# Optimization experiments

Measured on AMD Instinct MI355X. Metric: run time of the kernel, lower is better.

## Reference

```python
import jax, jax.numpy as jnp
import numpy as np


def setup_inputs() -> dict:
    key = jax.random.key(0)
    k1, k2 = jax.random.split(key)
    B, C, T = 8, 256, 2048
    n_q, bins = 8, 1024
    x = jax.random.normal(k1, (B, C, T), dtype=jnp.float32)
    codebook = jax.random.normal(k2, (n_q, bins, C), dtype=jnp.float32)
    return {"x": x, "codebook": codebook, "sample_rate": 24000, "bandwidth": 6}


def reference(x, codebook, sample_rate, bandwidth):
    B, C, T = x.shape
    n_q, bins, _ = codebook.shape
    # flatten frames: (B, C, T) -> (B*T, C)
    x_flat = jnp.transpose(x, (0, 2, 1)).reshape(-1, C)
    # the expanded (N, n_q, bins, C) subtraction, without materializing it)
    x2 = jnp.sum(x_flat * x_flat, axis=-1)[:, None, None]          # (N, 1, 1)
    c2 = jnp.sum(codebook * codebook, axis=-1)[None]               # (1, n_q, bins)
    xc = jnp.einsum('nd,qbd->nqb', x_flat, codebook)               # (N, n_q, bins)
    distances = x2 + c2 - 2.0 * xc
    indices = jnp.argmin(distances, axis=-1)                       # (N, n_q)
    # gather one code per quantizer level and sum (matches the python loop)
    gathered = codebook[jnp.arange(n_q)[None, :], indices]         # (N, n_q, C)
    quant_flat = jnp.sum(gathered, axis=1)                         # (N, C)
    quantized = jnp.transpose(quant_flat.reshape(B, T, C), (0, 2, 1))
    commitment_loss = jnp.mean((jax.lax.stop_gradient(quantized) - x) ** 2)
    codebook_loss = jnp.mean((quantized - jax.lax.stop_gradient(x)) ** 2)
    loss = commitment_loss + codebook_loss
    q_ste = x + jax.lax.stop_gradient(quantized - x)               # straight-through
    return q_ste, indices, loss
```

## Files before the change

### kernel.cpp

```cpp
#include <hip/hip_runtime.h>

typedef unsigned long long u64;
typedef unsigned int u32;
typedef _Float16 f16;
typedef f16 f16x8 __attribute__((ext_vector_type(8)));
typedef float f32x4 __attribute__((ext_vector_type(4)));

#define B_   8
#define C_   256
#define T_   2048
#define NQ   8
#define BINS 1024
#define NROWS (B_ * T_)
#define KA   256
#define KB   256
#define NTILE 16
#define MARGIN 3.0f

#define XS_OFF   ((size_t)0)
#define CS_OFF   ((size_t)8388608)
#define XT_OFF   ((size_t)12582912)
#define C2D_OFF  ((size_t)29360128)
#define C2K_OFF  ((size_t)29425664)
#define IDXI_OFF ((size_t)29458432)

static __device__ __forceinline__ void gll16(const void* g, void* l) {
    __builtin_amdgcn_global_load_lds(
        (const __attribute__((address_space(1))) u32*)g,
        (__attribute__((address_space(3))) u32*)l, 16, 0, 0);
}

__global__ __launch_bounds__(256)
void prep_x(const float* __restrict__ x, float* __restrict__ x_t,
            f16* __restrict__ xs) {
    __shared__ float tile[64][65];
    const int tid = threadIdx.x;
    const int bid = blockIdx.x;
    const int b  = bid >> 7;
    const int c0 = ((bid >> 5) & 3) * 64;
    const int t0 = (bid & 31) * 64;
    {
        const int j = tid & 63, cg = tid >> 6;
        #pragma unroll
        for (int ii = 0; ii < 16; ++ii) {
            const int cl = cg * 16 + ii;
            tile[cl][j] = x[((size_t)(b * C_ + c0 + cl) * T_) + t0 + j];
        }
    }
    __syncthreads();
    {
        const int cl = tid & 63, tg = tid >> 6;
        #pragma unroll
        for (int jj = 0; jj < 16; ++jj) {
            const int tl = tg * 16 + jj;
            const float v = tile[cl][tl];
            const size_t n = (size_t)b * T_ + t0 + tl;
            x_t[n * C_ + c0 + cl] = v;
            xs[n * KA + c0 + cl]  = (f16)v;
        }
    }
}

struct alignas(8) H4 { f16 v[4]; };
__global__ __launch_bounds__(256)
void prep_cb_c2(const float* __restrict__ cb, f16* __restrict__ cs,
                double* __restrict__ c2d, float* __restrict__ c2k) {
    const int w    = threadIdx.x >> 6;
    const int lane = threadIdx.x & 63;
    const int code = blockIdx.x * 4 + w;
    const float4 v = *(const float4*)(cb + (size_t)code * C_ + lane * 4);
    H4 h;
    h.v[0] = (f16)v.x; h.v[1] = (f16)v.y; h.v[2] = (f16)v.z; h.v[3] = (f16)v.w;
    *(H4*)(cs + (size_t)code * KB + lane * 4) = h;
    double s = (double)v.x * v.x + (double)v.y * v.y +
               (double)v.z * v.z + (double)v.w * v.w;
    #pragma unroll
    for (int off = 32; off; off >>= 1) s += __shfl_down(s, off, 64);
    if (lane == 0) {
        c2d[code] = s;
        c2k[code] = (float)s + 1000.0f;
    }
}

__global__ __launch_bounds__(512)
void dist_kernel(const f16* __restrict__ xs, const f16* __restrict__ cs,
                 const float* __restrict__ c2k, const float* __restrict__ x_t,
                 const float* __restrict__ cb, const double* __restrict__ c2d,
                 float* __restrict__ idx_f, int* __restrict__ idx_i) {
    __shared__ f16 Bs[2][64][256];
    __shared__ u32 red[128][8];

    const int tid  = threadIdx.x;
    const int lane = tid & 63;
    const int w    = tid >> 6;
    const int wr   = w >> 2;
    const int wc   = w & 3;
    const int bid  = blockIdx.x;
    const int q    = bid & 7;
    const int rt   = bid >> 3;
    const int n0   = rt * 128;

    const int c = lane & 15;
    const int g = lane >> 4;

    f16x8 af[4][8];
    {
        const f16* pa = xs + (size_t)(n0 + wr * 64 + c) * KA + g * 8;
        #pragma unroll
        for (int m = 0; m < 4; ++m)
            #pragma unroll
            for (int kk = 0; kk < 8; ++kk)
                af[m][kk] = *(const f16x8*)(pa + m * 16 * KA + kk * 32);
    }

    const int crow0 = tid >> 5;
    const int slotl = (tid & 31) ^ (crow0 & 7);
    const f16* srcb = cs + (size_t)q * 1024 * KB + (size_t)crow0 * KB
                         + slotl * 8;
    const int dstw = w * 512;

    #define STAGE(buf, t)                                                    \
        do {                                                                 \
            f16* b0 = &Bs[buf][0][0] + dstw;                                 \
            const f16* s_ = srcb + (size_t)(t) * 64 * KB;                    \
            gll16(s_,                 b0);                                   \
            gll16(s_ + 16 * KB,       b0 + 4096);                            \
            gll16(s_ + 32 * KB,       b0 + 8192);                            \
            gll16(s_ + 48 * KB,       b0 + 12288);                           \
        } while (0)

    u32 k1[4][4], k2[4][4];
    #pragma unroll
    for (int m = 0; m < 4; ++m)
        #pragma unroll
        for (int r = 0; r < 4; ++r) { k1[m][r] = ~0u; k2[m][r] = ~0u; }

    const float* c2q = c2k + q * BINS;
    const int rowoff = (wc * 16 + c) * 256;
    const int sw = c & 7;

    STAGE(0, 0);
    __syncthreads();

    #pragma unroll 1
    for (int t = 0; t < NTILE; ++t) {
        const int buf = t & 1;
        if (t < NTILE - 1) STAGE(buf ^ 1, t + 1);

        f32x4 acc[4];
        #pragma unroll
        for (int m = 0; m < 4; ++m) {
            f32x4 z = {0.f, 0.f, 0.f, 0.f};
            acc[m] = z;
        }

        const f16* bb = &Bs[buf][0][0] + rowoff;
        #pragma unroll
        for (int half = 0; half < 2; ++half) {
            f16x8 bg[4];
            #pragma unroll
            for (int k4 = 0; k4 < 4; ++k4) {
                const int kk = half * 4 + k4;
                bg[k4] = *(const f16x8*)(bb + ((kk * 4 + g) ^ sw) * 8);
            }
            #pragma unroll
            for (int k4 = 0; k4 < 4; ++k4)
                #pragma unroll
                for (int m = 0; m < 4; ++m)
                    acc[m] = __builtin_amdgcn_mfma_f32_16x16x32_f16(
                        af[m][half * 4 + k4], bg[k4], acc[m], 0, 0, 0);
        }

        const int codeL = t * 64 + wc * 16 + c;
        const float cc = c2q[codeL];
        #pragma unroll
        for (int m = 0; m < 4; ++m)
            #pragma unroll
            for (int r = 0; r < 4; ++r) {
                const float sc = fmaf(-2.f, acc[m][r], cc);
                const u32 key = (__float_as_uint(sc) & 0xFFFFFC00u) | (u32)codeL;
                const u32 hi = k1[m][r] > key ? k1[m][r] : key;
                k1[m][r] = k1[m][r] < key ? k1[m][r] : key;
                k2[m][r] = k2[m][r] < hi ? k2[m][r] : hi;
            }

        __syncthreads();
    }
    #undef STAGE

    #pragma unroll
    for (int m = 0; m < 4; ++m)
        #pragma unroll
        for (int r = 0; r < 4; ++r) {
            u32 a1 = k1[m][r], a2 = k2[m][r];
            #pragma unroll
            for (int mask = 1; mask <= 8; mask <<= 1) {
                const u32 o1 = __shfl_xor(a1, mask, 64);
                const u32 o2 = __shfl_xor(a2, mask, 64);
                const u32 hi = a1 > o1 ? a1 : o1;
                a1 = a1 < o1 ? a1 : o1;
                const u32 lo2 = o2 < a2 ? o2 : a2;
                a2 = hi < lo2 ? hi : lo2;
            }
            if (c == 0) {
                const int rowl = wr * 64 + m * 16 + g * 4 + r;
                red[rowl][wc * 2]     = a1;
                red[rowl][wc * 2 + 1] = a2;
            }
        }
    __syncthreads();

    if (tid < 128) {
        u32 s0 = ~0u, s1 = ~0u, s2 = ~0u, s3 = ~0u;
        #pragma unroll
        for (int jj = 0; jj < 8; ++jj) {
            const u32 k = red[tid][jj];
            if (k < s0)      { s3 = s2; s2 = s1; s1 = s0; s0 = k; }
            else if (k < s1) { s3 = s2; s2 = s1; s1 = k; }
            else if (k < s2) { s3 = s2; s2 = k; }
            else if (k < s3) { s3 = k; }
        }
        const float f0 = __uint_as_float(s0 & 0xFFFFFC00u);
        const float f1 = __uint_as_float(s1 & 0xFFFFFC00u);
        red[tid][0] = s0 & 1023u;
        red[tid][1] = s1 & 1023u;
        red[tid][2] = s2 & 1023u;
        red[tid][3] = s3 & 1023u;
        red[tid][4] = (f1 - f0 <= MARGIN) ? 1u : 0u;
    }
    __syncthreads();

    {
        const int cand = lane >> 4;
        const int cg   = lane & 15;
        #pragma unroll 1
        for (int i = 0; i < 16; ++i) {
            const int rl = w * 16 + i;
            const int n  = n0 + rl;
            if (!red[rl][4]) {
                if (lane == 0) {
                    const int win = (int)red[rl][0];
                    idx_f[(size_t)n * NQ + q] = (float)win;
                    idx_i[(size_t)n * NQ + q] = win;
                }
                continue;
            }
            const int bin = (int)red[rl][cand];
            const float* xr = x_t + (size_t)n * C_ + cg * 16;
            const float* cr = cb + ((size_t)(q * BINS + bin)) * C_ + cg * 16;
            double d = 0.0;
            #pragma unroll
            for (int u = 0; u < 4; ++u) {
                const float4 xv = *(const float4*)(xr + u * 4);
                const float4 cv = *(const float4*)(cr + u * 4);
                d += (double)xv.x * cv.x + (double)xv.y * cv.y
                   + (double)xv.z * cv.z + (double)xv.w * cv.w;
            }
            #pragma unroll
            for (int off = 8; off; off >>= 1) d += __shfl_down(d, off, 16);
            const double dist = c2d[q * BINS + bin] - 2.0 * d;
            const double d0 = __shfl(dist,  0, 64);
            const double d1 = __shfl(dist, 16, 64);
            const double d2 = __shfl(dist, 32, 64);
            const double d3 = __shfl(dist, 48, 64);
            if (lane == 0) {
                const int b0 = (int)red[rl][0], b1 = (int)red[rl][1];
                const int b2 = (int)red[rl][2], b3 = (int)red[rl][3];
                double best = d0;
                int win = b0;
                if (d1 < best || (d1 == best && b1 < win)) { best = d1; win = b1; }
                if (d2 < best || (d2 == best && b2 < win)) { best = d2; win = b2; }
                if (d3 < best || (d3 == best && b3 < win)) { best = d3; win = b3; }
                idx_f[(size_t)n * NQ + q] = (float)win;
                idx_i[(size_t)n * NQ + q] = win;
            }
        }
    }
}

__global__ __launch_bounds__(256)
void gather_kernel(const float* __restrict__ x, const float* __restrict__ cb,
                   const int* __restrict__ idx_i, float* __restrict__ out,
                   float* __restrict__ loss) {
    __shared__ float ql[C_][17];
    const int blk = blockIdx.x;
    const int b   = blk >> 7;
    const int t0  = (blk & 127) << 4;
    const int tid = threadIdx.x;
    {
        const int c = tid;
        for (int nl = 0; nl < 16; ++nl) {
            const int n = b * T_ + t0 + nl;
            float acc = 0.f;
            #pragma unroll
            for (int qq = 0; qq < NQ; ++qq) {
                const int id = idx_i[(size_t)n * NQ + qq];
                acc += cb[((size_t)qq * BINS + id) * C_ + c];
            }
            ql[c][nl] = acc;
        }
    }
    __syncthreads();
    const int tx = tid & 15, ty = tid >> 4;
    float lsum = 0.f;
    for (int cg = 0; cg < 16; ++cg) {
        const int c = cg * 16 + ty;
        const size_t off = ((size_t)b * C_ + c) * T_ + t0 + tx;
        const float qv = ql[c][tx];
        const float xv = x[off];
        out[off] = qv;
        const float d = qv - xv;
        lsum += d * d;
    }
    #pragma unroll
    for (int off = 32; off; off >>= 1) lsum += __shfl_down(lsum, off, 64);
    if ((tid & 63) == 0)
        atomicAdd(loss, lsum * (2.0f / (float)(B_ * C_ * T_)));
}

extern "C" void kernel_launch(void* const* d_in, const int* in_sizes, int n_in,
                              void* d_out, int out_size, void* d_ws, size_t ws_size,
                              hipStream_t stream) {
    const float* x  = (const float*)d_in[0];
    const float* cb = (const float*)d_in[1];

    float* out   = (float*)d_out;
    float* idx_f = out + (size_t)B_ * C_ * T_;
    float* loss  = idx_f + (size_t)NROWS * NQ;

    char* ws = (char*)d_ws;
    f16*    xs    = (f16*)(ws + XS_OFF);
    f16*    cs    = (f16*)(ws + CS_OFF);
    float*  x_t   = (float*)(ws + XT_OFF);
    double* c2d   = (double*)(ws + C2D_OFF);
    float*  c2k   = (float*)(ws + C2K_OFF);
    int*    idx_i = (int*)(ws + IDXI_OFF);

    hipMemsetAsync(loss, 0, sizeof(float), stream);
    prep_x<<<1024, 256, 0, stream>>>(x, x_t, xs);
    prep_cb_c2<<<2048, 256, 0, stream>>>(cb, cs, c2d, c2k);
    dist_kernel<<<1024, 512, 0, stream>>>(xs, cs, c2k, x_t, cb, c2d,
                                          idx_f, idx_i);
    gather_kernel<<<B_ * (T_ / 16), 256, 0, stream>>>(x, cb, idx_i, out, loss);
}
```

Measured before the change: 231.6 us.

## Make each dist block sweep all quantizers for 64 rows with wider code tiles

The distance kernel now gives each block 64 rows and loops over all 8 quantizers' codebooks (64 tiles of 128 codes), instead of one quantizer per block over 128 rows. The x fragment is loaded into registers once and reused across all quantizers, so there are fewer redundant A loads and fewer blocks (256). Per-quantizer top-2 results are flushed to a global scratch buffer instead of shared memory. The grid shrinks to 256 blocks with 8 waves each, which may underfill the GPU's CUs. The global round-trip for the reduction data relies on __syncthreads for visibility.

```diff
diff --git a/kernel.cpp b/kernel.cpp
--- a/kernel.cpp
+++ b/kernel.cpp
@@ -14,15 +14,16 @@
 #define NROWS (B_ * T_)
 #define KA   256
 #define KB   256
-#define NTILE 16
+#define TILES 64
 #define MARGIN 3.0f
 
 #define XS_OFF   ((size_t)0)
 #define CS_OFF   ((size_t)8388608)
 #define XT_OFF   ((size_t)12582912)
-#define C2D_OFF  ((size_t)29360128)
-#define C2K_OFF  ((size_t)29425664)
-#define IDXI_OFF ((size_t)29458432)
+#define RED_OFF  ((size_t)29360128)
+#define C2D_OFF  ((size_t)37748736)
+#define C2K_OFF  ((size_t)37814272)
+#define IDXI_OFF ((size_t)37847040)
 
 static __device__ __forceinline__ void gll16(const void* g, void* l) {
     __builtin_amdgcn_global_load_lds(
@@ -82,30 +83,26 @@
     }
 }
 
-__global__ __launch_bounds__(512)
+__global__ __launch_bounds__(512, 2)
 void dist_kernel(const f16* __restrict__ xs, const f16* __restrict__ cs,
                  const float* __restrict__ c2k, const float* __restrict__ x_t,
                  const float* __restrict__ cb, const double* __restrict__ c2d,
-                 float* __restrict__ idx_f, int* __restrict__ idx_i) {
-    __shared__ f16 Bs[2][64][256];
-    __shared__ u32 red[128][8];
+                 u32* __restrict__ red_g, float* __restrict__ idx_f,
+                 int* __restrict__ idx_i) {
+    __shared__ f16 Bs[2][128][256];
 
     const int tid  = threadIdx.x;
     const int lane = tid & 63;
     const int w    = tid >> 6;
-    const int wr   = w >> 2;
-    const int wc   = w & 3;
     const int bid  = blockIdx.x;
-    const int q    = bid & 7;
-    const int rt   = bid >> 3;
-    const int n0   = rt * 128;
+    const int n0   = bid * 64;
 
     const int c = lane & 15;
     const int g = lane >> 4;
 
     f16x8 af[4][8];
     {
-        const f16* pa = xs + (size_t)(n0 + wr * 64 + c) * KA + g * 8;
+        const f16* pa = xs + (size_t)(n0 + c) * KA + g * 8;
         #pragma unroll
         for (int m = 0; m < 4; ++m)
             #pragma unroll
@@ -115,18 +112,15 @@
 
     const int crow0 = tid >> 5;
     const int slotl = (tid & 31) ^ (crow0 & 7);
-    const f16* srcb = cs + (size_t)q * 1024 * KB + (size_t)crow0 * KB
-                         + slotl * 8;
-    const int dstw = w * 512;
+    const f16* srcb = cs + (size_t)crow0 * KB + slotl * 8;
 
     #define STAGE(buf, t)                                                    \
         do {                                                                 \
-            f16* b0 = &Bs[buf][0][0] + dstw;                                 \
-            const f16* s_ = srcb + (size_t)(t) * 64 * KB;                    \
-            gll16(s_,                 b0);                                   \
-            gll16(s_ + 16 * KB,       b0 + 4096);                            \
-            gll16(s_ + 32 * KB,       b0 + 8192);                            \
-            gll16(s_ + 48 * KB,       b0 + 12288);                           \
+            f16* b0 = &Bs[buf][0][0] + w * 512;                              \
+            const f16* s_ = srcb + (size_t)(t) * 128 * KB;                   \
+            _Pragma("unroll")                                                \
+            for (int i_ = 0; i_ < 8; ++i_)                                   \
+                gll16(s_ + (size_t)i_ * 16 * KB, b0 + i_ * 4096);            \
         } while (0)
 
     u32 k1[4][4], k2[4][4];
@@ -135,17 +129,16 @@
         #pragma unroll
         for (int r = 0; r < 4; ++r) { k1[m][r] = ~0u; k2[m][r] = ~0u; }
 
-    const float* c2q = c2k + q * BINS;
-    const int rowoff = (wc * 16 + c) * 256;
+    const int rowoff = (w * 16 + c) * 256;
     const int sw = c & 7;
 
     STAGE(0, 0);
     __syncthreads();
 
     #pragma unroll 1
-    for (int t = 0; t < NTILE; ++t) {
+    for (int t = 0; t < TILES; ++t) {
         const int buf = t & 1;
-        if (t < NTILE - 1) STAGE(buf ^ 1, t + 1);
+        if (t < TILES - 1) STAGE(buf ^ 1, t + 1);
 
         f32x4 acc[4];
         #pragma unroll
@@ -171,8 +164,8 @@
                         af[m][half * 4 + k4], bg[k4], acc[m], 0, 0, 0);
         }
 
-        const int codeL = t * 64 + wc * 16 + c;
-        const float cc = c2q[codeL];
+        const int codeL = (t & 7) * 128 + w * 16 + c;
+        const float cc = c2k[t * 128 + w * 16 + c];
         #pragma unroll
         for (int m = 0; m < 4; ++m)
             #pragma unroll
@@ -184,37 +177,43 @@
                 k2[m][r] = k2[m][r] < hi ? k2[m][r] : hi;
             }
 
+        if ((t & 7) == 7) {
+            const int q = t >> 3;
+            #pragma unroll
+            for (int m = 0; m < 4; ++m)
+                #pragma unroll
+                for (int r = 0; r < 4; ++r) {
+                    u32 a1 = k1[m][r], a2 = k2[m][r];
+                    #pragma unroll
+                    for (int mask = 1; mask <= 8; mask <<= 1) {
+                        const u32 o1 = __shfl_xor(a1, mask, 64);
+                        const u32 o2 = __shfl_xor(a2, mask, 64);
+                        const u32 hi = a1 > o1 ? a1 : o1;
+                        a1 = a1 < o1 ? a1 : o1;
+                        const u32 lo2 = o2 < a2 ? o2 : a2;
+                        a2 = hi < lo2 ? hi : lo2;
+                    }
+                    if (c == 0) {
+                        const int row = m * 16 + g * 4 + r;
+                        u64* dst = (u64*)(red_g +
+                            (((size_t)(bid * 8 + q) * 64 + row) * 16) + w * 2);
+                        *dst = (u64)a1 | ((u64)a2 << 32);
+                    }
+                    k1[m][r] = ~0u; k2[m][r] = ~0u;
+                }
+        }
+
         __syncthreads();
     }
     #undef STAGE
 
-    #pragma unroll
-    for (int m = 0; m < 4; ++m)
-        #pragma unroll
-        for (int r = 0; r < 4; ++r) {
-            u32 a1 = k1[m][r], a2 = k2[m][r];
-            #pragma unroll
-            for (int mask = 1; mask <= 8; mask <<= 1) {
-                const u32 o1 = __shfl_xor(a1, mask, 64);
-                const u32 o2 = __shfl_xor(a2, mask, 64);
-                const u32 hi = a1 > o1 ? a1 : o1;
-                a1 = a1 < o1 ? a1 : o1;
-                const u32 lo2 = o2 < a2 ? o2 : a2;
-                a2 = hi < lo2 ? hi : lo2;
-            }
-            if (c == 0) {
-                const int rowl = wr * 64 + m * 16 + g * 4 + r;
-                red[rowl][wc * 2]     = a1;
-                red[rowl][wc * 2 + 1] = a2;
-            }
-        }
-    __syncthreads();
-
-    if (tid < 128) {
+    {
+        const int q = tid >> 6, row = tid & 63;
+        volatile const u32* src = red_g + ((size_t)(bid * 8 + q) * 64 + row) * 16;
         u32 s0 = ~0u, s1 = ~0u, s2 = ~0u, s3 = ~0u;
         #pragma unroll
-        for (int jj = 0; jj < 8; ++jj) {
-            const u32 k = red[tid][jj];
+        for (int jj = 0; jj < 16; ++jj) {
+            const u32 k = src[jj];
             if (k < s0)      { s3 = s2; s2 = s1; s1 = s0; s0 = k; }
             else if (k < s1) { s3 = s2; s2 = s1; s1 = k; }
             else if (k < s2) { s3 = s2; s2 = k; }
@@ -222,30 +221,33 @@
         }
         const float f0 = __uint_as_float(s0 & 0xFFFFFC00u);
         const float f1 = __uint_as_float(s1 & 0xFFFFFC00u);
-        red[tid][0] = s0 & 1023u;
-        red[tid][1] = s1 & 1023u;
-        red[tid][2] = s2 & 1023u;
-        red[tid][3] = s3 & 1023u;
-        red[tid][4] = (f1 - f0 <= MARGIN) ? 1u : 0u;
+        u32* dst = red_g + ((size_t)(bid * 8 + q) * 64 + row) * 16;
+        dst[0] = s0 & 1023u;
+        dst[1] = s1 & 1023u;
+        dst[2] = s2 & 1023u;
+        dst[3] = s3 & 1023u;
+        dst[4] = (f1 - f0 <= MARGIN) ? 1u : 0u;
     }
     __syncthreads();
 
     {
+        const int q    = w;
         const int cand = lane >> 4;
         const int cg   = lane & 15;
         #pragma unroll 1
-        for (int i = 0; i < 16; ++i) {
-            const int rl = w * 16 + i;
-            const int n  = n0 + rl;
-            if (!red[rl][4]) {
+        for (int row = 0; row < 64; ++row) {
+            volatile const u32* base =
+                red_g + ((size_t)(bid * 8 + q) * 64 + row) * 16;
+            const int n = n0 + row;
+            if (!base[4]) {
                 if (lane == 0) {
-                    const int win = (int)red[rl][0];
+                    const int win = (int)base[0];
                     idx_f[(size_t)n * NQ + q] = (float)win;
                     idx_i[(size_t)n * NQ + q] = win;
                 }
                 continue;
             }
-            const int bin = (int)red[rl][cand];
+            const int bin = (int)base[cand];
             const float* xr = x_t + (size_t)n * C_ + cg * 16;
             const float* cr = cb + ((size_t)(q * BINS + bin)) * C_ + cg * 16;
             double d = 0.0;
@@ -264,8 +266,8 @@
             const double d2 = __shfl(dist, 32, 64);
             const double d3 = __shfl(dist, 48, 64);
             if (lane == 0) {
-                const int b0 = (int)red[rl][0], b1 = (int)red[rl][1];
-                const int b2 = (int)red[rl][2], b3 = (int)red[rl][3];
+                const int b0 = (int)base[0], b1 = (int)base[1];
+                const int b2 = (int)base[2], b3 = (int)base[3];
                 double best = d0;
                 int win = b0;
                 if (d1 < best || (d1 == best && b1 < win)) { best = d1; win = b1; }
@@ -332,6 +334,7 @@
     f16*    xs    = (f16*)(ws + XS_OFF);
     f16*    cs    = (f16*)(ws + CS_OFF);
     float*  x_t   = (float*)(ws + XT_OFF);
+    u32*    red_g = (u32*)(ws + RED_OFF);
     double* c2d   = (double*)(ws + C2D_OFF);
     float*  c2k   = (float*)(ws + C2K_OFF);
     int*    idx_i = (int*)(ws + IDXI_OFF);
@@ -339,7 +342,7 @@
     hipMemsetAsync(loss, 0, sizeof(float), stream);
     prep_x<<<1024, 256, 0, stream>>>(x, x_t, xs);
     prep_cb_c2<<<2048, 256, 0, stream>>>(cb, cs, c2d, c2k);
-    dist_kernel<<<1024, 512, 0, stream>>>(xs, cs, c2k, x_t, cb, c2d,
-                                          idx_f, idx_i);
+    dist_kernel<<<256, 512, 0, stream>>>(xs, cs, c2k, x_t, cb, c2d,
+                                         red_g, idx_f, idx_i);
     gather_kernel<<<B_ * (T_ / 16), 256, 0, stream>>>(x, cb, idx_i, out, loss);
 }
```

After: 264.9 us. 1.14x slower.
